# Optimization experiments

Measured on AMD Instinct MI355X. Metric: run time of the kernel, lower is better.

## Reference

```python
import jax, jax.numpy as jnp
import numpy as np

B, NMAX, H, DH, K = 16, 1024, 4, 32, 16
C = H * DH  # 128 = hidden_dim
T = 8192


def _dense_batch(feat, batch):
    # PyG to_dense_batch: [T, ...] + segment ids -> [B, NMAX, ...] + mask
    t = feat.shape[0]
    counts = jax.ops.segment_sum(jnp.ones((t,), jnp.int32), batch, num_segments=B)
    starts = jnp.concatenate([jnp.zeros((1,), jnp.int32), jnp.cumsum(counts)[:-1].astype(jnp.int32)])
    idx = jnp.arange(t) - starts[batch]
    dense = jnp.zeros((B, NMAX) + feat.shape[1:], feat.dtype).at[batch, idx].set(feat)
    mask = jnp.zeros((B, NMAX), bool).at[batch, idx].set(True)
    return dense, mask


def _forward(batch, x, pos, emb_W, emb_b, Wq, Wk, Wv0, Wv1, Wo0, Wo1, Wg, dist_scale, head_W, head_b):
    # 1) node embedding, then dense-batch (as in original forward)
    f0_flat = x @ emb_W + emb_b                      # [T, C]
    f0, mask = _dense_batch(f0_flat, batch)          # [B,N,C], [B,N]
    coords, _ = _dense_batch(pos, batch)             # [B,N,3]

    # 2) kNN graph from coordinates (num_neighbors=16, attend_self=True -> self is nearest)
    rel = coords[:, :, None, :] - coords[:, None, :, :]      # [B,N,N,3]
    d2 = jnp.sum(rel * rel, axis=-1)                         # [B,N,N]
    pv = mask[:, :, None] & mask[:, None, :]
    d2m = jnp.where(pv, d2, 1e9)
    _, nbr = jax.lax.top_k(-d2m, K)                          # [B,N,K]

    bidx = jnp.arange(B)[:, None, None]
    rel_n = jnp.take_along_axis(rel, nbr[..., None], axis=2)  # [B,N,K,3]
    d2_n = jnp.take_along_axis(d2, nbr, axis=2)               # [B,N,K]
    nbr_valid = jnp.take_along_axis(pv, nbr, axis=2)          # [B,N,K]
    dist = jnp.sqrt(d2_n + 1e-6)
    direc = rel_n / dist[..., None]                           # degree-1 spherical harmonic (unit rel dir)

    # 3) SE(3)-equivariant kNN attention (degree-0 and degree-1 outputs)
    q = (f0 @ Wq).reshape(B, NMAX, H, DH)
    k_n = (f0 @ Wk)[bidx, nbr].reshape(B, NMAX, K, H, DH)
    v0_n = (f0 @ Wv0)[bidx, nbr].reshape(B, NMAX, K, H, DH)
    v1_n = (f0 @ Wv1)[bidx, nbr].reshape(B, NMAX, K, H, DH)

    logits = jnp.einsum('bnhd,bnkhd->bnhk', q, k_n) / np.sqrt(DH)
    logits = logits - jax.nn.softplus(dist_scale)[None, None, :, None] * dist[:, :, None, :]
    logits = jnp.where(nbr_valid[:, :, None, :], logits, -1e9)
    attn = jax.nn.softmax(logits, axis=-1)                    # [B,N,H,K]

    out0 = jnp.einsum('bnhk,bnkhd->bnhd', attn, v0_n).reshape(B, NMAX, C)
    out1 = jnp.einsum('bnhk,bnkhd,bnkj->bnhdj', attn, v1_n, direc).reshape(B, NMAX, C, 3)

    # equivariant channel mixing of type-1, then invariant norm gates type-0 (residual)
    f1 = jnp.einsum('bncj,cd->bndj', out1, Wo1)               # [B,N,C,3]
    inv = jnp.sqrt(jnp.sum(f1 * f1, axis=-1) + 1e-6)          # [B,N,C]
    f0_out = f0 + out0 @ Wo0 + inv @ Wg

    # 4) masked mean pool over nodes + linear head
    mf = mask.astype(f0_out.dtype)
    pooled = jnp.sum(f0_out * mf[..., None], axis=1) / jnp.maximum(jnp.sum(mf, axis=1, keepdims=True), 1.0)
    return pooled @ head_W + head_b                           # [B, 19]


def setup_inputs() -> dict:
    key = jax.random.key(0)
    ks = jax.random.split(key, 16)
    def w(k, shape, fan_in):
        return jax.random.normal(k, shape, jnp.float32) / np.sqrt(fan_in)
    return {
        'x': jax.random.normal(ks[0], (T, 11), jnp.float32),
        'pos': jax.random.normal(ks[1], (T, 3), jnp.float32),
        'batch': jnp.sort(jax.random.randint(ks[2], (T,), 0, B)),
        'emb_W': w(ks[3], (11, C), 11), 'emb_b': jnp.zeros((C,), jnp.float32),
        'Wq': w(ks[4], (C, C), C), 'Wk': w(ks[5], (C, C), C),
        'Wv0': w(ks[6], (C, C), C), 'Wv1': w(ks[7], (C, C), C),
        'Wo0': w(ks[8], (C, C), C), 'Wo1': w(ks[9], (C, C), C),
        'Wg': w(ks[10], (C, C), C),
        'dist_scale': jax.random.normal(ks[11], (H,), jnp.float32) * 0.1,
        'head_W': w(ks[12], (C, 19), C), 'head_b': jnp.zeros((19,), jnp.float32),
    }


def reference(x, pos, batch, emb_W, emb_b, Wq, Wk, Wv0, Wv1, Wo0, Wo1, Wg, dist_scale, head_W, head_b):
    return _forward(batch, x, pos, emb_W, emb_b, Wq, Wk, Wv0, Wv1, Wo0, Wo1, Wg, dist_scale, head_W, head_b)
```

## Files before the change

### kernel.cpp

```cpp
#include <hip/hip_runtime.h>
#include <hip/hip_bf16.h>
#include <math.h>

#define T_NODES 8192
#define BGRAPHS 16
#define CDIM 128
#define HEADS 4
#define DHEAD 32
#define KNN 16

__device__ __forceinline__ void seg_probe(const int* __restrict__ batch, int t,
                                          int lane, int& s_out, int& n_out) {
    int b = batch[t];
    int pb = t - lane * 16;
    int qf = t + lane * 16;
    int vb = batch[pb < 0 ? 0 : pb];
    int vf = batch[qf > T_NODES - 1 ? T_NODES - 1 : qf];
    bool eqb = (pb >= 0) && (vb == b);
    bool eqf = (qf < T_NODES) && (vf == b);
    unsigned long long mb = __ballot(eqb);
    unsigned long long mf = __ballot(eqf);
    int m1 = (~mb == 0ULL) ? 64 : (int)__builtin_ctzll(~mb);
    int m2 = (~mf == 0ULL) ? 64 : (int)__builtin_ctzll(~mf);
    int wsb = (m1 == 64) ? (t - 1023) : (t - m1 * 16 + 1);
    int wsf = (m2 == 64) ? (t + 1009) : (t + (m2 - 1) * 16 + 1);
    int pos2 = (lane < 16) ? (wsb + lane) : (wsf + (lane - 16));
    int pc = pos2 < 0 ? 0 : (pos2 > T_NODES - 1 ? T_NODES - 1 : pos2);
    int v2 = batch[pc];
    bool cb = (lane < 16) && ((pos2 < 0) || (v2 < b));
    bool cf = (lane >= 16) && (lane < 32) && (pos2 < T_NODES) && (v2 == b);
    s_out = wsb + (int)__popcll(__ballot(cb));
    n_out = wsf + (int)__popcll(__ballot(cf)) - s_out;
}

template <int NS>
__device__ __forceinline__ void knn_body(const float* __restrict__ pos,
                                         int t, int s, int n, int lane,
                                         int* __restrict__ nbr,
                                         float4* __restrict__ dird) {
    float px = pos[t * 3 + 0], py = pos[t * 3 + 1], pz = pos[t * 3 + 2];
    float sd[NS];
    int ss[NS];
#pragma unroll
    for (int sl = 0; sl < NS; ++sl) {
        int j = lane + sl * 64;
        float d2 = 1e30f;
        if (j < n) {
            int jj = s + j;
            float dx = px - pos[jj * 3 + 0];
            float dy = py - pos[jj * 3 + 1];
            float dz = pz - pos[jj * 3 + 2];
            d2 = dx * dx + dy * dy + dz * dz;
        }
        sd[sl] = d2;
        ss[sl] = sl;
    }
#pragma unroll
    for (int p = 1; p < NS; p <<= 1) {
#pragma unroll
        for (int k = p; k >= 1; k >>= 1) {
#pragma unroll
            for (int j = (k & (p - 1)); j + k < NS; j += 2 * k) {
#pragma unroll
                for (int i = 0; i < k; ++i) {
                    if (i + j + k < NS && ((i + j) / (2 * p)) == ((i + j + k) / (2 * p))) {
                        int a = i + j, c2 = i + j + k;
                        bool sw = sd[a] > sd[c2];
                        float td = sd[a];
                        int ts = ss[a];
                        sd[a] = sw ? sd[c2] : sd[a];
                        ss[a] = sw ? ss[c2] : ss[a];
                        sd[c2] = sw ? td : sd[c2];
                        ss[c2] = sw ? ts : ss[c2];
                    }
                }
            }
        }
    }

    float resd = 1e30f;
    int resj = -1;
#pragma unroll
    for (int r = 0; r < KNN; ++r) {
        float rd = sd[0];
#pragma unroll
        for (int off = 32; off >= 1; off >>= 1) {
            rd = fminf(rd, __shfl_xor(rd, off));
        }
        unsigned long long mask = __ballot(sd[0] == rd);
        int wl = (int)__builtin_ctzll(mask);
        int ws = __shfl(ss[0], wl);
        if (lane == r) { resd = rd; resj = wl + ws * 64; }
        if (lane == wl) {
#pragma unroll
            for (int i = 0; i < NS - 1; ++i) { sd[i] = sd[i + 1]; ss[i] = ss[i + 1]; }
            sd[NS - 1] = 1e30f;
        }
    }

    if (lane < KNN) {
        bool valid = (resd < 1e29f);
        int jf = valid ? (s + resj) : -1;
        nbr[t * KNN + lane] = jf;
        float dd = sqrtf(resd + 1e-6f);
        float dx = 0.f, dy = 0.f, dz = 0.f;
        if (valid) {
            float inv = 1.f / dd;
            dx = (px - pos[jf * 3 + 0]) * inv;
            dy = (py - pos[jf * 3 + 1]) * inv;
            dz = (pz - pos[jf * 3 + 2]) * inv;
        }
        float4 v;
        v.x = dx; v.y = dy; v.z = dz; v.w = dd;
        dird[t * KNN + lane] = v;
    }
}

template <int NS>
__device__ __forceinline__ void knn_pair_body(const float* __restrict__ pos,
                                              int t, int s, int n, int lane,
                                              int* __restrict__ nbr,
                                              float4* __restrict__ dird) {
    int l32 = lane & 31;
    float px = pos[t * 3 + 0], py = pos[t * 3 + 1], pz = pos[t * 3 + 2];
    float sd[NS];
    int ss[NS];
#pragma unroll
    for (int sl = 0; sl < NS; ++sl) {
        int j = l32 + sl * 32;
        float d2 = 1e30f;
        if (j < n) {
            int jj = s + j;
            float dx = px - pos[jj * 3 + 0];
            float dy = py - pos[jj * 3 + 1];
            float dz = pz - pos[jj * 3 + 2];
            d2 = dx * dx + dy * dy + dz * dz;
        }
        sd[sl] = d2;
        ss[sl] = sl;
    }
#pragma unroll
    for (int p = 1; p < NS; p <<= 1) {
#pragma unroll
        for (int k = p; k >= 1; k >>= 1) {
#pragma unroll
            for (int j = (k & (p - 1)); j + k < NS; j += 2 * k) {
#pragma unroll
                for (int i = 0; i < k; ++i) {
                    if (i + j + k < NS && ((i + j) / (2 * p)) == ((i + j + k) / (2 * p))) {
                        int a = i + j, c2 = i + j + k;
                        bool sw = sd[a] > sd[c2];
                        float td = sd[a];
                        int ts = ss[a];
                        sd[a] = sw ? sd[c2] : sd[a];
                        ss[a] = sw ? ss[c2] : ss[a];
                        sd[c2] = sw ? td : sd[c2];
                        ss[c2] = sw ? ts : ss[c2];
                    }
                }
            }
        }
    }

    float resd = 1e30f;
    int resj = -1;
#pragma unroll
    for (int r = 0; r < KNN; ++r) {
        unsigned key = (__float_as_uint(sd[0]) & ~31u) | (unsigned)l32;
        key = min(key, (unsigned)__shfl_xor((int)key, 16));
        key = min(key, (unsigned)__shfl_xor((int)key, 8));
        key = min(key, (unsigned)__shfl_xor((int)key, 4));
        key = min(key, (unsigned)__shfl_xor((int)key, 2));
        key = min(key, (unsigned)__shfl_xor((int)key, 1));
        int wl32 = (int)(key & 31u);
        int wl = wl32 + (lane & 32);
        float rd = __shfl(sd[0], wl);
        int ws = __shfl(ss[0], wl);
        if (l32 == r) { resd = rd; resj = wl32 + ws * 32; }
        if (lane == wl) {
#pragma unroll
            for (int i = 0; i < NS - 1; ++i) { sd[i] = sd[i + 1]; ss[i] = ss[i + 1]; }
            sd[NS - 1] = 1e30f;
        }
    }

    if (l32 < KNN) {
        bool valid = (resd < 1e29f);
        int jf = valid ? (s + resj) : -1;
        nbr[t * KNN + l32] = jf;
        float dd = sqrtf(resd + 1e-6f);
        float dx = 0.f, dy = 0.f, dz = 0.f;
        if (valid) {
            float inv = 1.f / dd;
            dx = (px - pos[jf * 3 + 0]) * inv;
            dy = (py - pos[jf * 3 + 1]) * inv;
            dz = (pz - pos[jf * 3 + 2]) * inv;
        }
        float4 v;
        v.x = dx; v.y = dy; v.z = dz; v.w = dd;
        dird[t * KNN + l32] = v;
    }
}

__global__ __launch_bounds__(256) void k_par(const float* __restrict__ pos,
                                             const int* __restrict__ batch,
                                             const float* __restrict__ x,
                                             const float* __restrict__ embW,
                                             const float* __restrict__ embb,
                                             const float* __restrict__ Wq,
                                             const float* __restrict__ Wk,
                                             const float* __restrict__ Wv0,
                                             const float* __restrict__ Wv1,
                                             const float* __restrict__ Wo0,
                                             const float* __restrict__ Wg,
                                             const float* __restrict__ headW,
                                             int* __restrict__ nbr,
                                             float4* __restrict__ dird,
                                             float* __restrict__ qkvv,
                                             float* __restrict__ poolF0,
                                             float* __restrict__ H1,
                                             float* __restrict__ H2) {
    __shared__ float smem[CDIM * 20];
    int bid = blockIdx.x;
    int tid = threadIdx.x;

    if (bid >= 1536) {
        int m = bid - 1536;
        const float* W = m ? Wg : Wo0;
        float* H = m ? H2 : H1;
        for (int i = tid; i < CDIM * 19; i += 256) smem[i] = headW[i];
        __syncthreads();
        for (int i = tid; i < CDIM * 19; i += 256) {
            int c = i / 19, o = i - c * 19;
            float acc = 0.f;
#pragma unroll 8
            for (int d = 0; d < CDIM; ++d) acc += W[c * CDIM + d] * smem[d * 19 + o];
            H[i] = acc;
        }
        return;
    }

    int g = bid / 3, r = bid - g * 3;
    if (r == 2) {
        float (*sf)[CDIM] = (float (*)[CDIM])smem;
        int t0 = g * 16;
        {
            int col = tid & 127;
            int pr = tid >> 7;
            float ew[11];
#pragma unroll
            for (int i = 0; i < 11; ++i) ew[i] = embW[i * CDIM + col];
            float eb = embb[col];
            float acc_run = 0.f;
            int gprev = batch[t0 + pr * 8];
#pragma unroll
            for (int nn8 = 0; nn8 < 8; ++nn8) {
                int nn = pr * 8 + nn8;
                int t = t0 + nn;
                float acc = eb;
#pragma unroll
                for (int i = 0; i < 11; ++i) acc += x[t * 11 + i] * ew[i];
                sf[nn][col] = acc;
                int gb = batch[t];
                if (gb != gprev) {
                    atomicAdd(&poolF0[gprev * CDIM + col], acc_run);
                    acc_run = 0.f;
                    gprev = gb;
                }
                acc_run += acc;
            }
            atomicAdd(&poolF0[gprev * CDIM + col], acc_run);
        }
        __syncthreads();

        const float* W1 = (tid < 128) ? Wq : Wk;
        const float* W2 = (tid < 128) ? Wv0 : Wv1;
        int col = tid & 127;

        float acc1[16], acc2[16];
#pragma unroll
        for (int nn = 0; nn < 16; ++nn) { acc1[nn] = 0.f; acc2[nn] = 0.f; }

        for (int c0 = 0; c0 < CDIM; c0 += 8) {
            float w1[8], w2[8];
#pragma unroll
            for (int cc = 0; cc < 8; ++cc) {
                w1[cc] = W1[(c0 + cc) * CDIM + col];
                w2[cc] = W2[(c0 + cc) * CDIM + col];
            }
#pragma unroll
            for (int nn = 0; nn < 16; ++nn) {
                float4 fa = *(const float4*)&sf[nn][c0];
                float4 fb = *(const float4*)&sf[nn][c0 + 4];
                acc1[nn] += fa.x * w1[0] + fa.y * w1[1] + fa.z * w1[2] + fa.w * w1[3]
                          + fb.x * w1[4] + fb.y * w1[5] + fb.z * w1[6] + fb.w * w1[7];
                acc2[nn] += fa.x * w2[0] + fa.y * w2[1] + fa.z * w2[2] + fa.w * w2[3]
                          + fb.x * w2[4] + fb.y * w2[5] + fb.z * w2[6] + fb.w * w2[7];
            }
        }
#pragma unroll
        for (int nn = 0; nn < 16; ++nn) {
            qkvv[(size_t)(t0 + nn) * 512 + tid] = acc1[nn];
            qkvv[(size_t)(t0 + nn) * 512 + 256 + tid] = acc2[nn];
        }
        return;
    }

    int kidx = g * 2 + r;
    int wave = tid >> 6;
    int lane = tid & 63;
    int tA = kidx * 8 + wave * 2;
    int tB = tA + 1;

    int sA, nA, sB, nB;
    seg_probe(batch, tA, lane, sA, nA);
    seg_probe(batch, tB, lane, sB, nB);

    int nmax = nA > nB ? nA : nB;
    if (nmax <= 512) {
        int t = (lane < 32) ? tA : tB;
        int s = (lane < 32) ? sA : sB;
        int n = (lane < 32) ? nA : nB;
        knn_pair_body<16>(pos, t, s, n, lane, nbr, dird);
    } else {
        knn_body<16>(pos, tA, sA, nA, lane, nbr, dird);
        knn_body<16>(pos, tB, sB, nB, lane, nbr, dird);
    }
}

__global__ __launch_bounds__(256) void k_attn(const float* __restrict__ qkvv,
                                              const int* __restrict__ nbr,
                                              const float4* __restrict__ dird,
                                              const int* __restrict__ batch,
                                              const float* __restrict__ dist_scale,
                                              const float* __restrict__ Wo1,
                                              float* __restrict__ poolO0,
                                              float* __restrict__ poolInv) {
    __shared__ float  s_a[4][64];
    __shared__ float4 s_d[4][16];
    __shared__ int    s_j[4][16];
    __shared__ float  s_o1[4][CDIM][4];
    __shared__ float  s_part[CDIM][13];
    __shared__ int    s_gid[4];

    int bid = blockIdx.x;
    int swz = (bid & 7) * (T_NODES / 32) + (bid >> 3);
    int wave = threadIdx.x >> 6;
    int lane = threadIdx.x & 63;
    int t0 = swz * 4;
    int t = t0 + wave;

    if (threadIdx.x < 4) s_gid[threadIdx.x] = batch[t0 + threadIdx.x];

    int k = lane & 15;
    int h = lane >> 4;

    int j = nbr[t * KNN + k];
    float4 dv = dird[t * KNN + k];
    if (h == 0) { s_j[wave][k] = j; s_d[wave][k] = dv; }

    const float4* qv = (const float4*)&qkvv[(size_t)t * 512 + h * DHEAD];
    const float4* kv = (j >= 0) ? (const float4*)&qkvv[(size_t)j * 512 + 128 + h * DHEAD] : qv;
    float dot = 0.f;
#pragma unroll
    for (int i = 0; i < 8; ++i) {
        float4 a = qv[i], b2 = kv[i];
        dot += a.x * b2.x + a.y * b2.y + a.z * b2.z + a.w * b2.w;
    }
    float xs = dist_scale[h];
    float sp = (xs > 20.f) ? xs : log1pf(expf(xs));
    float lg = (j >= 0) ? (dot * 0.17677669529663687f - sp * dv.w) : -1e30f;

    float m = lg;
    m = fmaxf(m, __shfl_xor(m, 1));
    m = fmaxf(m, __shfl_xor(m, 2));
    m = fmaxf(m, __shfl_xor(m, 4));
    m = fmaxf(m, __shfl_xor(m, 8));
    float e = expf(lg - m);
    float ssum = e;
    ssum += __shfl_xor(ssum, 1);
    ssum += __shfl_xor(ssum, 2);
    ssum += __shfl_xor(ssum, 4);
    ssum += __shfl_xor(ssum, 8);
    s_a[wave][h * 16 + k] = e / ssum;

    __syncthreads();

    int c2 = lane * 2;
    int hh = lane >> 4;

    float o0x = 0.f, o0y = 0.f;
    float o1xx = 0.f, o1xy = 0.f;
    float o1yx = 0.f, o1yy = 0.f;
    float o1zx = 0.f, o1zy = 0.f;

#pragma unroll
    for (int kk = 0; kk < KNN; ++kk) {
        int jj = s_j[wave][kk];
        if (jj >= 0) {
            float a = s_a[wave][hh * 16 + kk];
            float4 d = s_d[wave][kk];
            float2 v0 = *(const float2*)&qkvv[(size_t)jj * 512 + 256 + c2];
            float2 v1 = *(const float2*)&qkvv[(size_t)jj * 512 + 384 + c2];
            o0x += a * v0.x;
            o0y += a * v0.y;
            float w1x = a * v1.x, w1y = a * v1.y;
            o1xx += w1x * d.x; o1xy += w1y * d.x;
            o1yx += w1x * d.y; o1yy += w1y * d.y;
            o1zx += w1x * d.z; o1zy += w1y * d.z;
        }
    }

    {
        float4 w0; w0.x = o1xx; w0.y = o1yx; w0.z = o1zx; w0.w = o0x;
        float4 w1; w1.x = o1xy; w1.y = o1yy; w1.z = o1zy; w1.w = o0y;
        *(float4*)&s_o1[wave][c2][0] = w0;
        *(float4*)&s_o1[wave][c2 + 1][0] = w1;
    }
    __syncthreads();

    int d = threadIdx.x & 127;
    int half = threadIdx.x >> 7;

    float acc[4][3];
#pragma unroll
    for (int nn = 0; nn < 4; ++nn) { acc[nn][0] = 0.f; acc[nn][1] = 0.f; acc[nn][2] = 0.f; }

    int cb0 = half * 64;
#pragma unroll 4
    for (int c = cb0; c < cb0 + 64; ++c) {
        float wv = Wo1[c * CDIM + d];
#pragma unroll
        for (int nn = 0; nn < 4; ++nn) {
            float4 v = *(const float4*)&s_o1[nn][c][0];
            acc[nn][0] += v.x * wv;
            acc[nn][1] += v.y * wv;
            acc[nn][2] += v.z * wv;
        }
    }
    if (half == 1) {
#pragma unroll
        for (int nn = 0; nn < 4; ++nn) {
            s_part[d][nn * 3 + 0] = acc[nn][0];
            s_part[d][nn * 3 + 1] = acc[nn][1];
            s_part[d][nn * 3 + 2] = acc[nn][2];
        }
    }
    __syncthreads();
    if (half == 0) {
        float accO = 0.f, accI = 0.f;
        int gprev = s_gid[0];
#pragma unroll
        for (int nn = 0; nn < 4; ++nn) {
            float fx = acc[nn][0] + s_part[d][nn * 3 + 0];
            float fy = acc[nn][1] + s_part[d][nn * 3 + 1];
            float fz = acc[nn][2] + s_part[d][nn * 3 + 2];
            float iv = sqrtf(fx * fx + fy * fy + fz * fz + 1e-6f);
            float o0v = s_o1[nn][d][3];
            int gb = s_gid[nn];
            if (gb != gprev) {
                atomicAdd(&poolO0[gprev * CDIM + d], accO);
                atomicAdd(&poolInv[gprev * CDIM + d], accI);
                accO = 0.f; accI = 0.f;
                gprev = gb;
            }
            accO += o0v;
            accI += iv;
        }
        atomicAdd(&poolO0[gprev * CDIM + d], accO);
        atomicAdd(&poolInv[gprev * CDIM + d], accI);
    }
}

__global__ __launch_bounds__(640) void k_pool(const float* __restrict__ poolF0,
                                              const float* __restrict__ poolO0,
                                              const float* __restrict__ poolInv,
                                              const int* __restrict__ batch,
                                              const float* __restrict__ headW,
                                              const float* __restrict__ H1,
                                              const float* __restrict__ H2,
                                              const float* __restrict__ headb,
                                              float* __restrict__ out) {
    __shared__ float P0[CDIM], P1[CDIM], P2[CDIM];
    int b = blockIdx.x;
    int tid = threadIdx.x;

    int lo = 0, hi = T_NODES;
    while (lo < hi) {
        int mid = (lo + hi) >> 1;
        bool lt = batch[mid] < b;
        lo = lt ? mid + 1 : lo;
        hi = lt ? hi : mid;
    }
    int s = lo;
    lo = 0; hi = T_NODES;
    while (lo < hi) {
        int mid = (lo + hi) >> 1;
        bool le = batch[mid] <= b;
        lo = le ? mid + 1 : lo;
        hi = le ? hi : mid;
    }
    int n = lo - s;
    float inv_n = 1.f / fmaxf((float)n, 1.f);

    if (tid < CDIM) {
        P0[tid] = poolF0[b * CDIM + tid] * inv_n;
        P1[tid] = poolO0[b * CDIM + tid] * inv_n;
        P2[tid] = poolInv[b * CDIM + tid] * inv_n;
    }
    __syncthreads();

    if (tid < 19 * 32) {
        int o = tid >> 5;
        int l = tid & 31;
        float p = 0.f;
#pragma unroll
        for (int cc = 0; cc < 4; ++cc) {
            int ch = l + cc * 32;
            p += P0[ch] * headW[ch * 19 + o]
               + P1[ch] * H1[ch * 19 + o]
               + P2[ch] * H2[ch * 19 + o];
        }
        p += __shfl_xor(p, 16);
        p += __shfl_xor(p, 8);
        p += __shfl_xor(p, 4);
        p += __shfl_xor(p, 2);
        p += __shfl_xor(p, 1);
        if (l == 0) out[b * 19 + o] = p + headb[o];
    }
}

extern "C" void kernel_launch(void* const* d_in, const int* in_sizes, int n_in,
                              void* d_out, int out_size, void* d_ws, size_t ws_size,
                              hipStream_t stream) {
    const float* x    = (const float*)d_in[0];
    const float* pos  = (const float*)d_in[1];
    const int* batch  = (const int*)d_in[2];
    const float* embW = (const float*)d_in[3];
    const float* embb = (const float*)d_in[4];
    const float* Wq   = (const float*)d_in[5];
    const float* Wk   = (const float*)d_in[6];
    const float* Wv0  = (const float*)d_in[7];
    const float* Wv1  = (const float*)d_in[8];
    const float* Wo0  = (const float*)d_in[9];
    const float* Wo1  = (const float*)d_in[10];
    const float* Wg   = (const float*)d_in[11];
    const float* dist_scale = (const float*)d_in[12];
    const float* headW = (const float*)d_in[13];
    const float* headb = (const float*)d_in[14];
    float* out = (float*)d_out;

    char* w = (char*)d_ws;
    float* qkvv = (float*)(w + 256);
    int* nbr    = (int*)(qkvv + (size_t)T_NODES * 512);
    float4* dird = (float4*)(nbr + (size_t)T_NODES * KNN);
    float* poolF0 = (float*)(dird + (size_t)T_NODES * KNN);
    float* poolO0 = poolF0 + BGRAPHS * CDIM;
    float* poolInv = poolO0 + BGRAPHS * CDIM;
    float* H1   = poolInv + BGRAPHS * CDIM;
    float* H2   = H1 + CDIM * 19;

    hipMemsetAsync(poolF0, 0, 3 * BGRAPHS * CDIM * sizeof(float), stream);
    k_par<<<1538, 256, 0, stream>>>(pos, batch, x, embW, embb, Wq, Wk, Wv0, Wv1,
                                    Wo0, Wg, headW, nbr, dird, qkvv, poolF0, H1, H2);
    k_attn<<<T_NODES / 4, 256, 0, stream>>>(qkvv, nbr, dird, batch, dist_scale, Wo1,
                                            poolO0, poolInv);
    k_pool<<<BGRAPHS, 640, 0, stream>>>(poolF0, poolO0, poolInv, batch, headW,
                                        H1, H2, headb, out);
}
```

Before: 113.2 us.

## Replace per-lane sort kNN with threshold-select and compact bitonic sort

```diff
diff --git a/kernel.cpp b/kernel.cpp
--- a/kernel.cpp
+++ b/kernel.cpp
@@ -116,15 +116,16 @@
     }
 }
 
-template <int NS>
-__device__ __forceinline__ void knn_pair_body(const float* __restrict__ pos,
-                                              int t, int s, int n, int lane,
-                                              int* __restrict__ nbr,
-                                              float4* __restrict__ dird) {
+__device__ __forceinline__ bool knn_tau(const float* __restrict__ pos,
+                                        int t, int s, int n, int lane,
+                                        float* __restrict__ ldsD,
+                                        int* __restrict__ ldsI,
+                                        int* __restrict__ nbr,
+                                        float4* __restrict__ dird) {
+    const int NS = 18;
     int l32 = lane & 31;
     float px = pos[t * 3 + 0], py = pos[t * 3 + 1], pz = pos[t * 3 + 2];
     float sd[NS];
-    int ss[NS];
 #pragma unroll
     for (int sl = 0; sl < NS; ++sl) {
         int j = l32 + sl * 32;
@@ -137,58 +138,65 @@
             d2 = dx * dx + dy * dy + dz * dz;
         }
         sd[sl] = d2;
-        ss[sl] = sl;
-    }
-#pragma unroll
-    for (int p = 1; p < NS; p <<= 1) {
-#pragma unroll
-        for (int k = p; k >= 1; k >>= 1) {
-#pragma unroll
-            for (int j = (k & (p - 1)); j + k < NS; j += 2 * k) {
-#pragma unroll
-                for (int i = 0; i < k; ++i) {
-                    if (i + j + k < NS && ((i + j) / (2 * p)) == ((i + j + k) / (2 * p))) {
-                        int a = i + j, c2 = i + j + k;
-                        bool sw = sd[a] > sd[c2];
-                        float td = sd[a];
-                        int ts = ss[a];
-                        sd[a] = sw ? sd[c2] : sd[a];
-                        ss[a] = sw ? ss[c2] : ss[a];
-                        sd[c2] = sw ? td : sd[c2];
-                        ss[c2] = sw ? ts : ss[c2];
-                    }
-                }
-            }
-        }
-    }
-
-    float resd = 1e30f;
-    int resj = -1;
-#pragma unroll
-    for (int r = 0; r < KNN; ++r) {
-        unsigned key = (__float_as_uint(sd[0]) & ~31u) | (unsigned)l32;
-        key = min(key, (unsigned)__shfl_xor((int)key, 16));
-        key = min(key, (unsigned)__shfl_xor((int)key, 8));
-        key = min(key, (unsigned)__shfl_xor((int)key, 4));
-        key = min(key, (unsigned)__shfl_xor((int)key, 2));
-        key = min(key, (unsigned)__shfl_xor((int)key, 1));
-        int wl32 = (int)(key & 31u);
-        int wl = wl32 + (lane & 32);
-        float rd = __shfl(sd[0], wl);
-        int ws = __shfl(ss[0], wl);
-        if (l32 == r) { resd = rd; resj = wl32 + ws * 32; }
-        if (lane == wl) {
-#pragma unroll
-            for (int i = 0; i < NS - 1; ++i) { sd[i] = sd[i + 1]; ss[i] = ss[i + 1]; }
-            sd[NS - 1] = 1e30f;
+    }
+    float v = sd[0];
+#pragma unroll
+    for (int sl = 1; sl < NS; ++sl) v = fminf(v, sd[sl]);
+#pragma unroll
+    for (int k = 2; k <= 32; k <<= 1) {
+#pragma unroll
+        for (int j = k >> 1; j > 0; j >>= 1) {
+            float o = __shfl_xor(v, j);
+            bool up = ((l32 & k) == 0);
+            bool lower = ((l32 & j) == 0);
+            v = (lower == up) ? fminf(v, o) : fmaxf(v, o);
+        }
+    }
+    float tau = __shfl(v, (lane & 32) + 15);
+
+    int cnt = 0;
+#pragma unroll
+    for (int sl = 0; sl < NS; ++sl) cnt += (sd[sl] <= tau) ? 1 : 0;
+    int pfx = cnt;
+#pragma unroll
+    for (int off = 1; off < 32; off <<= 1) {
+        int y = __shfl(pfx, lane - off);
+        if (l32 >= off) pfx += y;
+    }
+    int M = __shfl(pfx, (lane & 32) + 31);
+    if (__ballot(M > 32)) return false;
+
+    int wp = pfx - cnt;
+    float* bd = ldsD + (lane >> 5) * 32;
+    int* bi = ldsI + (lane >> 5) * 32;
+#pragma unroll
+    for (int sl = 0; sl < NS; ++sl) {
+        if (sd[sl] <= tau) { bd[wp] = sd[sl]; bi[wp] = l32 + sl * 32; ++wp; }
+    }
+    __asm__ volatile("s_waitcnt lgkmcnt(0)" ::: "memory");
+
+    float kd = (l32 < M) ? bd[l32] : 1e30f;
+    int ki = (l32 < M) ? bi[l32] : 0;
+#pragma unroll
+    for (int k = 2; k <= 32; k <<= 1) {
+#pragma unroll
+        for (int j = k >> 1; j > 0; j >>= 1) {
+            float od = __shfl_xor(kd, j);
+            int oi = __shfl_xor(ki, j);
+            bool up = ((l32 & k) == 0);
+            bool lower = ((l32 & j) == 0);
+            bool keepMin = (lower == up);
+            bool take = keepMin ? (od < kd) : (od > kd);
+            kd = keepMin ? fminf(kd, od) : fmaxf(kd, od);
+            ki = take ? oi : ki;
         }
     }
 
     if (l32 < KNN) {
-        bool valid = (resd < 1e29f);
-        int jf = valid ? (s + resj) : -1;
+        bool valid = (kd < 1e29f);
+        int jf = valid ? (s + ki) : -1;
         nbr[t * KNN + l32] = jf;
-        float dd = sqrtf(resd + 1e-6f);
+        float dd = sqrtf(kd + 1e-6f);
         float dx = 0.f, dy = 0.f, dz = 0.f;
         if (valid) {
             float inv = 1.f / dd;
@@ -196,10 +204,11 @@
             dy = (py - pos[jf * 3 + 1]) * inv;
             dz = (pz - pos[jf * 3 + 2]) * inv;
         }
-        float4 v;
-        v.x = dx; v.y = dy; v.z = dz; v.w = dd;
-        dird[t * KNN + l32] = v;
-    }
+        float4 vv;
+        vv.x = dx; vv.y = dy; vv.z = dz; vv.w = dd;
+        dird[t * KNN + l32] = vv;
+    }
+    return true;
 }
 
 __global__ __launch_bounds__(256) void k_par(const float* __restrict__ pos,
@@ -316,13 +325,18 @@
     seg_probe(batch, tA, lane, sA, nA);
     seg_probe(batch, tB, lane, sB, nB);
 
+    float* ldsD = smem + wave * 64;
+    int* ldsI = (int*)(smem + 256) + wave * 64;
+
     int nmax = nA > nB ? nA : nB;
-    if (nmax <= 512) {
+    bool done = false;
+    if (nmax <= 576) {
         int t = (lane < 32) ? tA : tB;
         int s = (lane < 32) ? sA : sB;
         int n = (lane < 32) ? nA : nB;
-        knn_pair_body<16>(pos, t, s, n, lane, nbr, dird);
-    } else {
+        done = knn_tau(pos, t, s, n, lane, ldsD, ldsI, nbr, dird);
+    }
+    if (!done) {
         knn_body<16>(pos, tA, sA, nA, lane, nbr, dird);
         knn_body<16>(pos, tB, sB, nB, lane, nbr, dird);
     }
```

Measured after the change: 112.2 us. About the same (-0.9%).
